# Optimization experiments

Measured on AMD Instinct MI355X. Metric: run time of the kernel, lower is better.

The kernel has to match this reference:

```python
import jax, jax.numpy as jnp
import numpy as np
from jax import lax

B, T, E, H, L, V = 64, 512, 512, 1024, 2, 32000  # batch, seq, d_emb, d_hid, n_layer, n_vocab


def setup_inputs() -> dict:
    key = jax.random.key(0)
    ks = jax.random.split(key, 8)
    s = 0.03  # small init keeps tanh recurrence well-conditioned
    return {
        "src": jax.random.randint(ks[0], (B, T), 0, V),
        "emb_table": jax.random.normal(ks[1], (V, E), jnp.float32) * s,
        "W1": jax.random.normal(ks[2], (H, E), jnp.float32) * s,
        "b1": jnp.zeros((H,), jnp.float32),
        "W2": jax.random.normal(ks[3], (H, H), jnp.float32) * s,
        "b2": jnp.zeros((H,), jnp.float32),
        # layer 0 input dim = H; layers >0 input dim = 2H (bidirectional concat)
        "W_ih0": jax.random.normal(ks[4], (2, H, H), jnp.float32) * s,
        "W_ihL": jax.random.normal(ks[5], (L - 1, 2, H, 2 * H), jnp.float32) * s,
        "W_hh": jax.random.normal(ks[6], (L, 2, H, H), jnp.float32) * s,
        "b_ih": jnp.zeros((L, 2, H), jnp.float32),
        "b_hh": jnp.zeros((L, 2, H), jnp.float32),
    }


def _rnn_dir(x, Wih, Whh, bih, bhh, reverse):
    # x: [B, T, Din]. Precompute input projection as one big GEMM, then scan.
    pre = jnp.einsum('bti,hi->tbh', x, Wih) + bih  # [T, B, H]

    def step(h, p):
        h = jnp.tanh(p + h @ Whh.T + bhh)
        return h, h

    h0 = jnp.zeros((x.shape[0], Whh.shape[0]), x.dtype)
    hT, hs = lax.scan(step, h0, pre, reverse=reverse)
    return hT, jnp.transpose(hs, (1, 0, 2))  # final state [B,H], outputs [B,T,H]


def reference(src, emb_table, W1, b1, W2, b2, W_ih0, W_ihL, W_hh, b_ih, b_hh):
    # Embedding with padding_idx=0 (row zeroed)
    table = emb_table.at[0].set(0.0)
    x = table[src]  # [B, T, E]
    # emb_to_hid MLP (dropout is identity in eval mode)
    x = jax.nn.relu(x @ W1.T + b1)
    x = jax.nn.relu(x @ W2.T + b2)  # [B, T, H]
    finals = []
    inp = x
    for l in range(L):
        Wih = W_ih0 if l == 0 else W_ihL[l - 1]
        hf, of = _rnn_dir(inp, Wih[0], W_hh[l, 0], b_ih[l, 0], b_hh[l, 0], False)
        hb, ob = _rnn_dir(inp, Wih[1], W_hh[l, 1], b_ih[l, 1], b_hh[l, 1], True)
        finals += [hf, hb]
        inp = jnp.concatenate([of, ob], axis=-1)  # [B, T, 2H]
    # torch h_n layout: [n_layer * num_directions, B, H], layer-major, dir-minor
    return jnp.stack(finals, axis=0)
```

## Files before the change

kernel.cpp:

```cpp
#include <hip/hip_runtime.h>


typedef _Float16 f16;
typedef _Float16 f16x8 __attribute__((ext_vector_type(8)));
typedef _Float16 f16x4 __attribute__((ext_vector_type(4)));
typedef float f32x4 __attribute__((ext_vector_type(4)));

static const size_t MB_ = 1024ull * 1024ull;
static const size_t OFF_X0    = 0;
static const size_t OFF_X1    = 64 * MB_;
static const size_t OFF_EMB   = OFF_X1;
static const size_t OFF_MLP1  = 96 * MB_;
static const size_t OFF_H     = 192 * MB_;
static const size_t OFF_FLAGS = 192 * MB_ + 512 * 1024;
static const size_t OFF_BIAS  = 192 * MB_ + 576 * 1024;
static const size_t OFF_W1C   = 193 * MB_;
static const size_t OFF_W2C   = 194 * MB_;
static const size_t WS_NEED   = 196 * MB_;
static const size_t Q_X0     = 0;
static const size_t Q_EMB    = 64 * MB_;
static const size_t Q_MLP1   = 96 * MB_;
static const size_t Q_W1C    = 160 * MB_;
static const size_t Q_W2C    = 161 * MB_;
static const size_t Q_PRE0D0 = 64 * MB_;
static const size_t Q_PRE0D1 = 128 * MB_;
static const size_t Q_HB0    = 192 * MB_;
static const size_t Q_FL0    = 192 * MB_ + 512 * 1024;
static const size_t Q_BIAS0  = 192 * MB_ + 544 * 1024;
static const size_t Q_PRE1D0 = 0;
static const size_t Q_PRE1D1 = 192 * MB_;
static const size_t Q_HB1    = 64 * MB_;
static const size_t Q_FL1    = 64 * MB_ + 512 * 1024;
static const size_t Q_BIAS1  = 64 * MB_ + 544 * 1024;
static const size_t WS_NEED2 = 256 * MB_;

__device__ __forceinline__ void gld16(const void* g, void* l) {
#if __has_builtin(__builtin_amdgcn_global_load_lds)
  __builtin_amdgcn_global_load_lds((const __attribute__((address_space(1))) void*)g,
                                   (__attribute__((address_space(3))) void*)l, 16, 0, 0);
#else
  *(f16x8*)l = *(const f16x8*)g;
#endif
}

__device__ __forceinline__ float tanh_fast(float x) {
  float ax = __builtin_fabsf(x);
  float e = __builtin_amdgcn_exp2f(ax * 2.8853900817779268f);
  float r = 1.0f - 2.0f * __builtin_amdgcn_rcpf(e + 1.0f);
  return __builtin_copysignf(r, x);
}


__global__ void zero_k(unsigned int* __restrict__ p, int n) {
  int i = blockIdx.x * blockDim.x + threadIdx.x;
  if (i < n) p[i] = 0u;
}

__global__ void cvt_k(const float* __restrict__ in, f16* __restrict__ out, int n4) {
  int i = blockIdx.x * blockDim.x + threadIdx.x;
  int stride = gridDim.x * blockDim.x;
  for (; i < n4; i += stride) {
    float4 v = ((const float4*)in)[i];
    f16x4 o = {(f16)v.x, (f16)v.y, (f16)v.z, (f16)v.w};
    ((f16x4*)out)[i] = o;
  }
}

__global__ void bias_k(const float* __restrict__ a, const float* __restrict__ b, float* __restrict__ o) {
  int i = blockIdx.x * blockDim.x + threadIdx.x;
  if (i < 4096) o[i] = a[i] + b[i];
}

__global__ void embed_k(const int* __restrict__ src, const float* __restrict__ tab, f16* __restrict__ out) {
  int m = blockIdx.x;
  int tid = threadIdx.x;
  int tok = src[m];
  f16x4 o = {(f16)0.f, (f16)0.f, (f16)0.f, (f16)0.f};
  if (tok != 0) {
    float4 v = *(const float4*)(tab + (size_t)tok * 512 + tid * 4);
    o[0] = (f16)v.x; o[1] = (f16)v.y; o[2] = (f16)v.z; o[3] = (f16)v.w;
  }
  *(f16x4*)(out + (size_t)m * 512 + tid * 4) = o;
}

template <int EPI>
__global__ __launch_bounds__(256) void gemm_f16(
    const f16* __restrict__ A, int lda, const f16* __restrict__ Bw,
    f16* __restrict__ out, const float* __restrict__ bias, int M, int N, int K) {
  __shared__ alignas(16) f16 As[4096];
  __shared__ alignas(16) f16 Bs[4096];
  const int nt = N >> 7;
  const int bx = blockIdx.x;
  const int tm = bx / nt, tn = bx - tm * nt;
  const int tid = threadIdx.x;
  const int l = tid & 63, w = tid >> 6;
  const int wr = w >> 1, wc = w & 1;
  const int srow = (w << 4) + (l >> 2);
  const int scol = (l & 3) << 3;
  const f16* Ab = A + (size_t)(tm * 128 + srow) * lda + scol;
  const f16* Bb = Bw + (size_t)(tn * 128 + srow) * K + scol;
  f32x4 acc[4][4];
#pragma unroll
  for (int i = 0; i < 4; i++)
#pragma unroll
    for (int j = 0; j < 4; j++) acc[i][j] = (f32x4){0.f, 0.f, 0.f, 0.f};
  const int ar = l & 15, ak = (l >> 4) << 3;
  for (int k0 = 0; k0 < K; k0 += 32) {
    gld16(Ab + k0, &As[tid * 8]);
    gld16(Ab + (size_t)64 * lda + k0, &As[tid * 8 + 2048]);
    gld16(Bb + k0, &Bs[tid * 8]);
    gld16(Bb + (size_t)64 * K + k0, &Bs[tid * 8 + 2048]);
    __syncthreads();
    f16x8 av[4], bv[4];
#pragma unroll
    for (int i = 0; i < 4; i++) av[i] = *(const f16x8*)&As[(wr * 64 + i * 16 + ar) * 32 + ak];
#pragma unroll
    for (int j = 0; j < 4; j++) bv[j] = *(const f16x8*)&Bs[(wc * 64 + j * 16 + ar) * 32 + ak];
#pragma unroll
    for (int i = 0; i < 4; i++)
#pragma unroll
      for (int j = 0; j < 4; j++)
        acc[i][j] = __builtin_amdgcn_mfma_f32_16x16x32_f16(av[i], bv[j], acc[i][j], 0, 0, 0);
    __syncthreads();
  }
  const int r0 = (l >> 4) << 2, c0 = l & 15;
#pragma unroll
  for (int i = 0; i < 4; i++) {
#pragma unroll
    for (int j = 0; j < 4; j++) {
      const int col = tn * 128 + wc * 64 + j * 16 + c0;
      const float bc = (EPI & 1) ? bias[col] : 0.f;
#pragma unroll
      for (int r = 0; r < 4; r++) {
        const int row = tm * 128 + wr * 64 + i * 16 + r0 + r;
        float v = acc[i][j][r];
        if (EPI & 1) { v += bc; v = v > 0.f ? v : 0.f; }
        if (EPI & 2) {
          const int b_ = row >> 9, t = row & 511;
          out[((size_t)(t * 64 + b_) << 10) + col] = (f16)v;
        } else {
          out[(size_t)row * N + col] = (f16)v;
        }
      }
    }
  }
}

__global__ __launch_bounds__(256) void gemm_b32(
    const f16* __restrict__ A, int lda, const float* __restrict__ Bw,
    f16* __restrict__ out, int M, int N, int K) {
  __shared__ alignas(16) f16 As[4096];
  __shared__ alignas(16) f16 Bs[4096];
  const int nt = N >> 7;
  const int bx = blockIdx.x;
  const int tm = bx / nt, tn = bx - tm * nt;
  const int tid = threadIdx.x;
  const int l = tid & 63, w = tid >> 6;
  const int wr = w >> 1, wc = w & 1;
  const int srow = (w << 4) + (l >> 2);
  const int scol = (l & 3) << 3;
  const f16* Ab = A + (size_t)(tm * 128 + srow) * lda + scol;
  const int brow = tid >> 1, bcol = (tid & 1) << 4;
  const float* Bb = Bw + (size_t)(tn * 128 + brow) * K + bcol;
  f32x4 acc[4][4];
#pragma unroll
  for (int i = 0; i < 4; i++)
#pragma unroll
    for (int j = 0; j < 4; j++) acc[i][j] = (f32x4){0.f, 0.f, 0.f, 0.f};
  const int ar = l & 15, ak = (l >> 4) << 3;
  for (int k0 = 0; k0 < K; k0 += 32) {
    gld16(Ab + k0, &As[tid * 8]);
    gld16(Ab + (size_t)64 * lda + k0, &As[tid * 8 + 2048]);
    {
      const float* bp = Bb + k0;
      float4 u0 = *(const float4*)(bp + 0), u1 = *(const float4*)(bp + 4);
      float4 u2 = *(const float4*)(bp + 8), u3 = *(const float4*)(bp + 12);
      f16x8 h0 = {(f16)u0.x, (f16)u0.y, (f16)u0.z, (f16)u0.w,
                  (f16)u1.x, (f16)u1.y, (f16)u1.z, (f16)u1.w};
      f16x8 h1 = {(f16)u2.x, (f16)u2.y, (f16)u2.z, (f16)u2.w,
                  (f16)u3.x, (f16)u3.y, (f16)u3.z, (f16)u3.w};
      *(f16x8*)&Bs[brow * 32 + bcol] = h0;
      *(f16x8*)&Bs[brow * 32 + bcol + 8] = h1;
    }
    __syncthreads();
    f16x8 av[4], bv[4];
#pragma unroll
    for (int i = 0; i < 4; i++) av[i] = *(const f16x8*)&As[(wr * 64 + i * 16 + ar) * 32 + ak];
#pragma unroll
    for (int j = 0; j < 4; j++) bv[j] = *(const f16x8*)&Bs[(wc * 64 + j * 16 + ar) * 32 + ak];
#pragma unroll
    for (int i = 0; i < 4; i++)
#pragma unroll
      for (int j = 0; j < 4; j++)
        acc[i][j] = __builtin_amdgcn_mfma_f32_16x16x32_f16(av[i], bv[j], acc[i][j], 0, 0, 0);
    __syncthreads();
  }
  const int r0 = (l >> 4) << 2, c0 = l & 15;
#pragma unroll
  for (int i = 0; i < 4; i++) {
#pragma unroll
    for (int j = 0; j < 4; j++) {
      const int col = tn * 128 + wc * 64 + j * 16 + c0;
#pragma unroll
      for (int r = 0; r < 4; r++) {
        const int row = tm * 128 + wr * 64 + i * 16 + r0 + r;
        out[(size_t)row * N + col] = (f16)acc[i][j][r];
      }
    }
  }
}

__global__ __launch_bounds__(256) void gemm_b32c(
    const f16* __restrict__ A0, const f16* __restrict__ A1, const float* __restrict__ Bw,
    f16* __restrict__ out, int M, int N) {
  constexpr int K = 2048;
  __shared__ alignas(16) f16 As[4096];
  __shared__ alignas(16) f16 Bs[4096];
  const int nt = N >> 7;
  const int bx = blockIdx.x;
  const int tm = bx / nt, tn = bx - tm * nt;
  const int tid = threadIdx.x;
  const int l = tid & 63, w = tid >> 6;
  const int wr = w >> 1, wc = w & 1;
  const int srow = (w << 4) + (l >> 2);
  const int scol = (l & 3) << 3;
  const int brow = tid >> 1, bcol = (tid & 1) << 4;
  const float* Bb = Bw + (size_t)(tn * 128 + brow) * K + bcol;
  f32x4 acc[4][4];
#pragma unroll
  for (int i = 0; i < 4; i++)
#pragma unroll
    for (int j = 0; j < 4; j++) acc[i][j] = (f32x4){0.f, 0.f, 0.f, 0.f};
  const int ar = l & 15, ak = (l >> 4) << 3;
  for (int k0 = 0; k0 < K; k0 += 32) {
    const f16* base = (k0 < 1024) ? A0 : A1;
    const int ko = k0 & 1023;
    const f16* Ab = base + (size_t)(tm * 128 + srow) * 1024 + ko + scol;
    gld16(Ab, &As[tid * 8]);
    gld16(Ab + (size_t)64 * 1024, &As[tid * 8 + 2048]);
    {
      const float* bp = Bb + k0;
      float4 u0 = *(const float4*)(bp + 0), u1 = *(const float4*)(bp + 4);
      float4 u2 = *(const float4*)(bp + 8), u3 = *(const float4*)(bp + 12);
      f16x8 h0 = {(f16)u0.x, (f16)u0.y, (f16)u0.z, (f16)u0.w,
                  (f16)u1.x, (f16)u1.y, (f16)u1.z, (f16)u1.w};
      f16x8 h1 = {(f16)u2.x, (f16)u2.y, (f16)u2.z, (f16)u2.w,
                  (f16)u3.x, (f16)u3.y, (f16)u3.z, (f16)u3.w};
      *(f16x8*)&Bs[brow * 32 + bcol] = h0;
      *(f16x8*)&Bs[brow * 32 + bcol + 8] = h1;
    }
    __syncthreads();
    f16x8 av[4], bv[4];
#pragma unroll
    for (int i = 0; i < 4; i++) av[i] = *(const f16x8*)&As[(wr * 64 + i * 16 + ar) * 32 + ak];
#pragma unroll
    for (int j = 0; j < 4; j++) bv[j] = *(const f16x8*)&Bs[(wc * 64 + j * 16 + ar) * 32 + ak];
#pragma unroll
    for (int i = 0; i < 4; i++)
#pragma unroll
      for (int j = 0; j < 4; j++)
        acc[i][j] = __builtin_amdgcn_mfma_f32_16x16x32_f16(av[i], bv[j], acc[i][j], 0, 0, 0);
    __syncthreads();
  }
  const int r0 = (l >> 4) << 2, c0 = l & 15;
#pragma unroll
  for (int i = 0; i < 4; i++) {
#pragma unroll
    for (int j = 0; j < 4; j++) {
      const int col = tn * 128 + wc * 64 + j * 16 + c0;
#pragma unroll
      for (int r = 0; r < 4; r++) {
        const int row = tm * 128 + wr * 64 + i * 16 + r0 + r;
        out[(size_t)row * N + col] = (f16)acc[i][j][r];
      }
    }
  }
}

template <int LAYER>
__global__ __launch_bounds__(512, 1) void rnn_scan(
    const f16* __restrict__ X, const float* __restrict__ Wih, const float* __restrict__ Whh,
    const float* __restrict__ bsum, f16* __restrict__ hbuf, unsigned int* __restrict__ flags,
    f16* __restrict__ seqout, float* __restrict__ dout) {
  constexpr int KX = LAYER ? 2048 : 1024;
  constexpr int XSH = LAYER ? 11 : 10;
  constexpr int NKX = KX / 128;
  constexpr int NKH = 8;
  const int bid = blockIdx.x;
  const int g_ = (bid & 7) >> 1;
  const int dir = g_ >> 1, bg = g_ & 1;
  const int cg = ((bid & 1) << 5) | (bid >> 3);
  const int tid = threadIdx.x, l = tid & 63, w = tid >> 6;
  const int mi = w & 1, kq = w >> 1;
  __shared__ alignas(16) f16 Wl[16 * 1024];
  __shared__ alignas(16) f16 Wi[16 * KX];
  __shared__ f32x4 part[2][4][64];
  __shared__ alignas(16) f16 p2[32][16];
  __shared__ unsigned int cnt;
  const int ld = LAYER * 2 + dir;
  if (tid == 0) cnt = 0u;
  for (int ch = tid; ch < 2048; ch += 512) {
    const int n = ch >> 7, k0 = (ch & 127) << 3;
    const float* wp = Whh + (((size_t)(ld * 1024 + cg * 16 + n)) << 10) + k0;
    float4 v0 = *(const float4*)wp, v1 = *(const float4*)(wp + 4);
    f16x8 hv = {(f16)v0.x, (f16)v0.y, (f16)v0.z, (f16)v0.w,
                (f16)v1.x, (f16)v1.y, (f16)v1.z, (f16)v1.w};
    *(f16x8*)&Wl[(n << 10) + (k0 ^ ((n & 7) << 3))] = hv;
  }
  for (int ch = tid; ch < (16 * KX / 8); ch += 512) {
    const int n = ch >> (XSH - 3), k0 = (ch & (KX / 8 - 1)) << 3;
    const float* wp = Wih + ((size_t)(dir * 1024 + cg * 16 + n)) * KX + k0;
    float4 v0 = *(const float4*)wp, v1 = *(const float4*)(wp + 4);
    f16x8 hv = {(f16)v0.x, (f16)v0.y, (f16)v0.z, (f16)v0.w,
                (f16)v1.x, (f16)v1.y, (f16)v1.z, (f16)v1.w};
    *(f16x8*)&Wi[(n << XSH) + (k0 ^ ((n & 7) << 3))] = hv;
  }
  const float bn = bsum[(ld << 10) + cg * 16 + (l & 15)];
  f16* hD = hbuf + ((size_t)dir << 17);
  unsigned int* fl = flags + ((dir * 2 + bg) << 10);
  const int arow = bg * 32 + mi * 16 + (l & 15);
  const int akh = (kq << 8) + ((l >> 4) << 3);
  const int akx = kq * (KX / 4) + ((l >> 4) << 3);
  const int wn = l & 15;
  const int wsw = (wn & 7) << 3;

  f16x8 xv[NKX];
  {
    const int t0 = dir ? 511 : 0;
    const f16* xr = X + (((size_t)(t0 * 64 + arow)) << XSH) + akx;
#pragma unroll
    for (int i = 0; i < NKX; i++)
      asm volatile("global_load_dwordx4 %0, %1, off offset:%2"
                   : "=&v"(xv[i]) : "v"(xr), "i"(64 * i));
  }
  __syncthreads();

  for (int s = 0; s < 512; ++s) {
    const int t = dir ? (511 - s) : s;
    f32x4 acc = {0.f, 0.f, 0.f, 0.f};
    if (s > 0) {
      if (w == 7) {
        const unsigned int tgt = (unsigned int)(LAYER * 512 + s);
        unsigned int* fp = fl + l * 16;
        for (;;) {
          unsigned int f = __hip_atomic_load(fp, __ATOMIC_RELAXED, __HIP_MEMORY_SCOPE_AGENT);
          if (__all((int)(f >= tgt))) break;
        }
      }
      __syncthreads();
      const f16* hrow = hD + (((size_t)(s & 1)) << 16) + (((size_t)arow) << 10) + akh;
      f16x8 hv[NKH];
#pragma unroll
      for (int i = 0; i < NKH; i++)
        asm volatile("global_load_dwordx4 %0, %1, off offset:%2 sc0 sc1"
                     : "=&v"(hv[i]) : "v"(hrow), "i"(64 * i));
      asm volatile("s_waitcnt vmcnt(%0)" :: "i"(NKH) : "memory");
      __builtin_amdgcn_sched_barrier(0);
#pragma unroll
      for (int it = 0; it < NKX; ++it) {
        const int ko = akx + it * 32;
        f16x8 bv = *(const f16x8*)&Wi[(wn << XSH) + (ko ^ wsw)];
        acc = __builtin_amdgcn_mfma_f32_16x16x32_f16(xv[it], bv, acc, 0, 0, 0);
      }
      asm volatile("s_waitcnt vmcnt(0)" ::: "memory");
      __builtin_amdgcn_sched_barrier(0);
#pragma unroll
      for (int it = 0; it < NKH; ++it) {
        const int ko = akh + it * 32;
        f16x8 bv = *(const f16x8*)&Wl[(wn << 10) + (ko ^ wsw)];
        acc = __builtin_amdgcn_mfma_f32_16x16x32_f16(hv[it], bv, acc, 0, 0, 0);
      }
    } else {
      asm volatile("s_waitcnt vmcnt(0)" ::: "memory");
      __builtin_amdgcn_sched_barrier(0);
#pragma unroll
      for (int it = 0; it < NKX; ++it) {
        const int ko = akx + it * 32;
        f16x8 bv = *(const f16x8*)&Wi[(wn << XSH) + (ko ^ wsw)];
        acc = __builtin_amdgcn_mfma_f32_16x16x32_f16(xv[it], bv, acc, 0, 0, 0);
      }
    }
    part[mi][kq][l] = acc;
    __syncthreads();
    if (w < 2) {
      f32x4 sum = part[w][0][l];
      sum += part[w][1][l];
      sum += part[w][2][l];
      sum += part[w][3][l];
#pragma unroll
      for (int r = 0; r < 4; ++r) {
        const int row = ((l >> 4) << 2) + r;
        float v = tanh_fast(sum[r] + bn);
        p2[(w << 4) + row][l & 15] = (f16)v;
        if (s == 511) {
          const int b_ = bg * 32 + (w << 4) + row;
          dout[(((size_t)(ld * 64 + b_)) << 10) + cg * 16 + (l & 15)] = v;
        }
      }
      asm volatile("s_waitcnt lgkmcnt(0)" ::: "memory");
      __builtin_amdgcn_sched_barrier(0);
      if (l < 32) {
        const int rr = (w << 4) + (l >> 1), hf = l & 1;
        f16x8 pv = *(const f16x8*)&p2[rr][hf * 8];
        const int b_ = bg * 32 + rr;
        f16* hp = hD + (((size_t)((s + 1) & 1)) << 16) + (((size_t)b_) << 10) + cg * 16 + hf * 8;
        asm volatile("global_store_dwordx4 %0, %1, off sc0 sc1" :: "v"(hp), "v"(pv) : "memory");
        if (LAYER == 0) {
          f16* sp = seqout + (((size_t)(t * 64 + b_)) << 11) + (dir << 10) + cg * 16 + hf * 8;
          asm volatile("global_store_dwordx4 %0, %1, off" :: "v"(sp), "v"(pv) : "memory");
        }
      }
      asm volatile("s_waitcnt vmcnt(0)" ::: "memory");
      __builtin_amdgcn_sched_barrier(0);
      if (l == 0) {
        unsigned int old = __hip_atomic_fetch_add(&cnt, 1u, __ATOMIC_RELAXED,
                                                  __HIP_MEMORY_SCOPE_WORKGROUP);
        if (old == (unsigned int)(2 * s + 1))
          __hip_atomic_store(&fl[cg * 16], (unsigned int)(LAYER * 512 + s + 1),
                             __ATOMIC_RELAXED, __HIP_MEMORY_SCOPE_AGENT);
      }
    }
    if (s + 1 < 512) {
      const int tn_ = dir ? (511 - (s + 1)) : (s + 1);
      const f16* xr = X + (((size_t)(tn_ * 64 + arow)) << XSH) + akx;
#pragma unroll
      for (int i = 0; i < NKX; i++)
        asm volatile("global_load_dwordx4 %0, %1, off offset:%2"
                     : "=&v"(xv[i]) : "v"(xr), "i"(64 * i));
    }
  }
}

template <int LAYER>
__global__ __launch_bounds__(512, 1) void rnn_scan_pre(
    f16* __restrict__ PRE0, f16* __restrict__ PRE1,
    const float* __restrict__ Whh, const float* __restrict__ bsum,
    f16* __restrict__ hbuf, unsigned int* __restrict__ flags,
    float* __restrict__ dout) {
  constexpr int NKH = 8;
  const int bid = blockIdx.x;
  const int g_ = (bid & 7) >> 1;
  const int dir = g_ >> 1, bg = g_ & 1;
  const int cg = ((bid & 1) << 5) | (bid >> 3);
  const int tid = threadIdx.x, l = tid & 63, w = tid >> 6;
  const int mi = w & 1, kq = w >> 1;
  __shared__ alignas(16) f16 Wl[16 * 1024];
  __shared__ f32x4 part[2][4][64];
  __shared__ alignas(16) f16 p2[32][16];
  __shared__ unsigned int cnt;
  const int ld = LAYER * 2 + dir;
  if (tid == 0) cnt = 0u;
  for (int ch = tid; ch < 2048; ch += 512) {
    const int n = ch >> 7, k0 = (ch & 127) << 3;
    const float* wp = Whh + (((size_t)(ld * 1024 + cg * 16 + n)) << 10) + k0;
    float4 v0 = *(const float4*)wp, v1 = *(const float4*)(wp + 4);
    f16x8 hv = {(f16)v0.x, (f16)v0.y, (f16)v0.z, (f16)v0.w,
                (f16)v1.x, (f16)v1.y, (f16)v1.z, (f16)v1.w};
    *(f16x8*)&Wl[(n << 10) + (k0 ^ ((n & 7) << 3))] = hv;
  }
  const int pcol = cg * 16 + (l & 15);
  const float bn = bsum[(ld << 10) + pcol];
  f16* preD = dir ? PRE1 : PRE0;
  f16* hD = hbuf + ((size_t)dir << 17);
  unsigned int* fl = flags + ((dir * 2 + bg) << 10);
  const int arow = bg * 32 + mi * 16 + (l & 15);
  const int akh = (kq << 8) + ((l >> 4) << 3);
  const int wn = l & 15;
  const int wsw = (wn & 7) << 3;
  const int prow = bg * 32 + (w << 4) + ((l >> 4) << 2);

  unsigned int pu0 = 0, pu1 = 0, pu2 = 0, pu3 = 0;
  if (w < 2) {
    const int t0 = dir ? 511 : 0;
    const f16* ppA = preD + (((size_t)(t0 * 64 + prow)) << 10) + pcol;
    const f16* ppB = ppA + 2048;
    asm volatile("global_load_ushort %0, %1, off" : "=&v"(pu0) : "v"(ppA));
    asm volatile("global_load_ushort %0, %1, off offset:2048" : "=&v"(pu1) : "v"(ppA));
    asm volatile("global_load_ushort %0, %1, off" : "=&v"(pu2) : "v"(ppB));
    asm volatile("global_load_ushort %0, %1, off offset:2048" : "=&v"(pu3) : "v"(ppB));
  }
  __syncthreads();

  for (int s = 0; s < 512; ++s) {
    const int t = dir ? (511 - s) : s;
    f32x4 acc = {0.f, 0.f, 0.f, 0.f};
    if (s > 0) {
      if (w == 7) {
        const unsigned int tgt = (unsigned int)s;
        unsigned int* fp = fl + l * 16;
        for (;;) {
          unsigned int f = __hip_atomic_load(fp, __ATOMIC_RELAXED, __HIP_MEMORY_SCOPE_AGENT);
          if (__all((int)(f >= tgt))) break;
        }
      }
      __syncthreads();
      const f16* hrow = hD + (((size_t)(s & 1)) << 16) + (((size_t)arow) << 10) + akh;
      f16x8 hv[NKH];
#pragma unroll
      for (int i = 0; i < NKH; i++)
        asm volatile("global_load_dwordx4 %0, %1, off offset:%2 sc0 sc1"
                     : "=&v"(hv[i]) : "v"(hrow), "i"(64 * i));
      asm volatile("s_waitcnt vmcnt(0)" ::: "memory");
      __builtin_amdgcn_sched_barrier(0);
#pragma unroll
      for (int it = 0; it < NKH; ++it) {
        const int ko = akh + it * 32;
        f16x8 bv = *(const f16x8*)&Wl[(wn << 10) + (ko ^ wsw)];
        acc = __builtin_amdgcn_mfma_f32_16x16x32_f16(hv[it], bv, acc, 0, 0, 0);
      }
    }
    part[mi][kq][l] = acc;
    __syncthreads();
    if (w < 2) {
      asm volatile("s_waitcnt vmcnt(0)" ::: "memory");
      __builtin_amdgcn_sched_barrier(0);
      float pva[4];
      pva[0] = (float)__builtin_bit_cast(f16, (unsigned short)pu0);
      pva[1] = (float)__builtin_bit_cast(f16, (unsigned short)pu1);
      pva[2] = (float)__builtin_bit_cast(f16, (unsigned short)pu2);
      pva[3] = (float)__builtin_bit_cast(f16, (unsigned short)pu3);
      f32x4 sum = part[w][0][l];
      sum += part[w][1][l];
      sum += part[w][2][l];
      sum += part[w][3][l];
#pragma unroll
      for (int r = 0; r < 4; ++r) {
        const int row = ((l >> 4) << 2) + r;
        float v = tanh_fast(sum[r] + pva[r] + bn);
        p2[(w << 4) + row][l & 15] = (f16)v;
        if (s == 511) {
          const int b_ = bg * 32 + (w << 4) + row;
          dout[(((size_t)(ld * 64 + b_)) << 10) + pcol] = v;
        }
      }
      asm volatile("s_waitcnt lgkmcnt(0)" ::: "memory");
      __builtin_amdgcn_sched_barrier(0);
      if (l < 32) {
        const int rr = (w << 4) + (l >> 1), hf = l & 1;
        f16x8 pv = *(const f16x8*)&p2[rr][hf * 8];
        const int b_ = bg * 32 + rr;
        f16* hp = hD + (((size_t)((s + 1) & 1)) << 16) + (((size_t)b_) << 10) + cg * 16 + hf * 8;
        asm volatile("global_store_dwordx4 %0, %1, off sc0 sc1" :: "v"(hp), "v"(pv) : "memory");
        if (LAYER == 0) {
          f16* xp = preD + (((size_t)(t * 64 + b_)) << 10) + cg * 16 + hf * 8;
          asm volatile("global_store_dwordx4 %0, %1, off" :: "v"(xp), "v"(pv) : "memory");
        }
      }
      asm volatile("s_waitcnt vmcnt(0)" ::: "memory");
      __builtin_amdgcn_sched_barrier(0);
      if (l == 0) {
        unsigned int old = __hip_atomic_fetch_add(&cnt, 1u, __ATOMIC_RELAXED,
                                                  __HIP_MEMORY_SCOPE_WORKGROUP);
        if (old == (unsigned int)(2 * s + 1))
          __hip_atomic_store(&fl[cg * 16], (unsigned int)(s + 1),
                             __ATOMIC_RELAXED, __HIP_MEMORY_SCOPE_AGENT);
      }
      if (s + 1 < 512) {
        const int tn_ = dir ? (511 - (s + 1)) : (s + 1);
        const f16* ppA = preD + (((size_t)(tn_ * 64 + prow)) << 10) + pcol;
        const f16* ppB = ppA + 2048;
        asm volatile("global_load_ushort %0, %1, off" : "=&v"(pu0) : "v"(ppA));
        asm volatile("global_load_ushort %0, %1, off offset:2048" : "=&v"(pu1) : "v"(ppA));
        asm volatile("global_load_ushort %0, %1, off" : "=&v"(pu2) : "v"(ppB));
        asm volatile("global_load_ushort %0, %1, off offset:2048" : "=&v"(pu3) : "v"(ppB));
      }
    }
  }
}


extern "C" void kernel_launch(void* const* d_in, const int* in_sizes, int n_in,
                              void* d_out, int out_size, void* d_ws, size_t ws_size,
                              hipStream_t stream) {
  const int* src    = (const int*)d_in[0];
  const float* emb  = (const float*)d_in[1];
  const float* W1   = (const float*)d_in[2];
  const float* b1   = (const float*)d_in[3];
  const float* W2   = (const float*)d_in[4];
  const float* b2   = (const float*)d_in[5];
  const float* Wih0 = (const float*)d_in[6];
  const float* WihL = (const float*)d_in[7];
  const float* Whh  = (const float*)d_in[8];
  const float* bih  = (const float*)d_in[9];
  const float* bhh  = (const float*)d_in[10];
  float* out = (float*)d_out;
  char* ws = (char*)d_ws;

  if (ws_size < WS_NEED) {
    zero_k<<<(out_size + 255) / 256, 256, 0, stream>>>((unsigned int*)d_out, out_size);
    return;
  }

  if (ws_size >= WS_NEED2) {
    f16* X0    = (f16*)(ws + Q_X0);
    f16* EMB   = (f16*)(ws + Q_EMB);
    f16* MLP1  = (f16*)(ws + Q_MLP1);
    f16* W1C   = (f16*)(ws + Q_W1C);
    f16* W2C   = (f16*)(ws + Q_W2C);
    f16* PRE0D0 = (f16*)(ws + Q_PRE0D0);
    f16* PRE0D1 = (f16*)(ws + Q_PRE0D1);
    f16* HB0   = (f16*)(ws + Q_HB0);
    unsigned int* FL0 = (unsigned int*)(ws + Q_FL0);
    float* BIAS0 = (float*)(ws + Q_BIAS0);
    f16* PRE1D0 = (f16*)(ws + Q_PRE1D0);
    f16* PRE1D1 = (f16*)(ws + Q_PRE1D1);
    f16* HB1   = (f16*)(ws + Q_HB1);
    unsigned int* FL1 = (unsigned int*)(ws + Q_FL1);
    float* BIAS1 = (float*)(ws + Q_BIAS1);

    cvt_k<<<256, 256, 0, stream>>>(W1, W1C, 131072);
    cvt_k<<<256, 256, 0, stream>>>(W2, W2C, 262144);

    embed_k<<<32768, 128, 0, stream>>>(src, emb, EMB);
    gemm_f16<1><<<2048, 256, 0, stream>>>(EMB, 512, W1C, MLP1, b1, 32768, 1024, 512);
    gemm_f16<3><<<2048, 256, 0, stream>>>(MLP1, 1024, W2C, X0, b2, 32768, 1024, 1024);

    gemm_b32<<<2048, 256, 0, stream>>>(X0, 1024, Wih0, PRE0D0, 32768, 1024, 1024);
    gemm_b32<<<2048, 256, 0, stream>>>(X0, 1024, Wih0 + (1u << 20), PRE0D1, 32768, 1024, 1024);
    zero_k<<<16, 256, 0, stream>>>(FL0, 4096);
    bias_k<<<16, 256, 0, stream>>>(bih, bhh, BIAS0);
    rnn_scan_pre<0><<<256, 512, 0, stream>>>(PRE0D0, PRE0D1, Whh, BIAS0, HB0, FL0, out);

    gemm_b32c<<<2048, 256, 0, stream>>>(PRE0D0, PRE0D1, WihL, PRE1D0, 32768, 1024);
    gemm_b32c<<<2048, 256, 0, stream>>>(PRE0D0, PRE0D1, WihL + (1u << 21), PRE1D1, 32768, 1024);
    zero_k<<<16, 256, 0, stream>>>(FL1, 4096);
    bias_k<<<16, 256, 0, stream>>>(bih, bhh, BIAS1);
    rnn_scan_pre<1><<<256, 512, 0, stream>>>(PRE1D0, PRE1D1, Whh, BIAS1, HB1, FL1, out);
    return;
  }

  f16* X0   = (f16*)(ws + OFF_X0);
  f16* X1   = (f16*)(ws + OFF_X1);
  f16* EMB  = (f16*)(ws + OFF_EMB);
  f16* MLP1 = (f16*)(ws + OFF_MLP1);
  f16* HB   = (f16*)(ws + OFF_H);
  unsigned int* FLAGS = (unsigned int*)(ws + OFF_FLAGS);
  float* BIAS = (float*)(ws + OFF_BIAS);
  f16* W1C  = (f16*)(ws + OFF_W1C);
  f16* W2C  = (f16*)(ws + OFF_W2C);

  cvt_k<<<256, 256, 0, stream>>>(W1, W1C, 131072);
  cvt_k<<<256, 256, 0, stream>>>(W2, W2C, 262144);
  bias_k<<<16, 256, 0, stream>>>(bih, bhh, BIAS);
  zero_k<<<16, 256, 0, stream>>>(FLAGS, 4096);

  embed_k<<<32768, 128, 0, stream>>>(src, emb, EMB);
  gemm_f16<1><<<2048, 256, 0, stream>>>(EMB, 512, W1C, MLP1, b1, 32768, 1024, 512);
  gemm_f16<3><<<2048, 256, 0, stream>>>(MLP1, 1024, W2C, X0, b2, 32768, 1024, 1024);

  rnn_scan<0><<<256, 512, 0, stream>>>(X0, Wih0, Whh, BIAS, HB, FLAGS, X1, out);
  rnn_scan<1><<<256, 512, 0, stream>>>(X1, WihL, Whh, BIAS, HB, FLAGS, nullptr, out);
}
```

Measured before the change: 4.999 ms.

## Drop K-split in recurrent scan: two waves compute full K, no LDS reduction

The recurrent scan kernel moves from 8 waves that split the K dimension four ways, with a shared-memory partial-sum reduction, to 4 waves where only two compute the full 1024-wide dot product. Each of those two waves issues all 32 hidden-state loads up front and consumes them in staged waits. This removes the LDS partial write, one block barrier and the reduction from each serial step. In exchange, the per-step MFMA chain per wave is four times longer and register pressure rises from holding 32 f16x8 vectors.

```diff
diff --git a/kernel.cpp b/kernel.cpp
--- a/kernel.cpp
+++ b/kernel.cpp
@@ -432,25 +432,22 @@
 }
 
 template <int LAYER>
-__global__ __launch_bounds__(512, 1) void rnn_scan_pre(
+__global__ __launch_bounds__(256, 1) void rnn_scan_pre(
     f16* __restrict__ PRE0, f16* __restrict__ PRE1,
     const float* __restrict__ Whh, const float* __restrict__ bsum,
     f16* __restrict__ hbuf, unsigned int* __restrict__ flags,
     float* __restrict__ dout) {
-  constexpr int NKH = 8;
   const int bid = blockIdx.x;
   const int g_ = (bid & 7) >> 1;
   const int dir = g_ >> 1, bg = g_ & 1;
   const int cg = ((bid & 1) << 5) | (bid >> 3);
   const int tid = threadIdx.x, l = tid & 63, w = tid >> 6;
-  const int mi = w & 1, kq = w >> 1;
   __shared__ alignas(16) f16 Wl[16 * 1024];
-  __shared__ f32x4 part[2][4][64];
   __shared__ alignas(16) f16 p2[32][16];
   __shared__ unsigned int cnt;
   const int ld = LAYER * 2 + dir;
   if (tid == 0) cnt = 0u;
-  for (int ch = tid; ch < 2048; ch += 512) {
+  for (int ch = tid; ch < 2048; ch += 256) {
     const int n = ch >> 7, k0 = (ch & 127) << 3;
     const float* wp = Whh + (((size_t)(ld * 1024 + cg * 16 + n)) << 10) + k0;
     float4 v0 = *(const float4*)wp, v1 = *(const float4*)(wp + 4);
@@ -463,8 +460,8 @@
   f16* preD = dir ? PRE1 : PRE0;
   f16* hD = hbuf + ((size_t)dir << 17);
   unsigned int* fl = flags + ((dir * 2 + bg) << 10);
-  const int arow = bg * 32 + mi * 16 + (l & 15);
-  const int akh = (kq << 8) + ((l >> 4) << 3);
+  const int arow = bg * 32 + (w << 4) + (l & 15);
+  const int kb = (l >> 4) << 3;
   const int wn = l & 15;
   const int wsw = (wn & 7) << 3;
   const int prow = bg * 32 + (w << 4) + ((l >> 4) << 2);
@@ -485,7 +482,7 @@
     const int t = dir ? (511 - s) : s;
     f32x4 acc = {0.f, 0.f, 0.f, 0.f};
     if (s > 0) {
-      if (w == 7) {
+      if (w == 3) {
         const unsigned int tgt = (unsigned int)s;
         unsigned int* fp = fl + l * 16;
         for (;;) {
@@ -494,23 +491,47 @@
         }
       }
       __syncthreads();
-      const f16* hrow = hD + (((size_t)(s & 1)) << 16) + (((size_t)arow) << 10) + akh;
-      f16x8 hv[NKH];
-#pragma unroll
-      for (int i = 0; i < NKH; i++)
-        asm volatile("global_load_dwordx4 %0, %1, off offset:%2 sc0 sc1"
-                     : "=&v"(hv[i]) : "v"(hrow), "i"(64 * i));
-      asm volatile("s_waitcnt vmcnt(0)" ::: "memory");
-      __builtin_amdgcn_sched_barrier(0);
-#pragma unroll
-      for (int it = 0; it < NKH; ++it) {
-        const int ko = akh + it * 32;
-        f16x8 bv = *(const f16x8*)&Wl[(wn << 10) + (ko ^ wsw)];
-        acc = __builtin_amdgcn_mfma_f32_16x16x32_f16(hv[it], bv, acc, 0, 0, 0);
-      }
-    }
-    part[mi][kq][l] = acc;
-    __syncthreads();
+      if (w < 2) {
+        const f16* hrow = hD + (((size_t)(s & 1)) << 16) + (((size_t)arow) << 10) + kb;
+        f16x8 hv[32];
+#pragma unroll
+        for (int i = 0; i < 32; i++)
+          asm volatile("global_load_dwordx4 %0, %1, off offset:%2 sc0 sc1"
+                       : "=&v"(hv[i]) : "v"(hrow), "i"(64 * i));
+        asm volatile("s_waitcnt vmcnt(24)" ::: "memory");
+        __builtin_amdgcn_sched_barrier(0);
+#pragma unroll
+        for (int it = 0; it < 8; ++it) {
+          const int ko = kb + it * 32;
+          f16x8 bv = *(const f16x8*)&Wl[(wn << 10) + (ko ^ wsw)];
+          acc = __builtin_amdgcn_mfma_f32_16x16x32_f16(hv[it], bv, acc, 0, 0, 0);
+        }
+        asm volatile("s_waitcnt vmcnt(16)" ::: "memory");
+        __builtin_amdgcn_sched_barrier(0);
+#pragma unroll
+        for (int it = 8; it < 16; ++it) {
+          const int ko = kb + it * 32;
+          f16x8 bv = *(const f16x8*)&Wl[(wn << 10) + (ko ^ wsw)];
+          acc = __builtin_amdgcn_mfma_f32_16x16x32_f16(hv[it], bv, acc, 0, 0, 0);
+        }
+        asm volatile("s_waitcnt vmcnt(8)" ::: "memory");
+        __builtin_amdgcn_sched_barrier(0);
+#pragma unroll
+        for (int it = 16; it < 24; ++it) {
+          const int ko = kb + it * 32;
+          f16x8 bv = *(const f16x8*)&Wl[(wn << 10) + (ko ^ wsw)];
+          acc = __builtin_amdgcn_mfma_f32_16x16x32_f16(hv[it], bv, acc, 0, 0, 0);
+        }
+        asm volatile("s_waitcnt vmcnt(0)" ::: "memory");
+        __builtin_amdgcn_sched_barrier(0);
+#pragma unroll
+        for (int it = 24; it < 32; ++it) {
+          const int ko = kb + it * 32;
+          f16x8 bv = *(const f16x8*)&Wl[(wn << 10) + (ko ^ wsw)];
+          acc = __builtin_amdgcn_mfma_f32_16x16x32_f16(hv[it], bv, acc, 0, 0, 0);
+        }
+      }
+    }
     if (w < 2) {
       asm volatile("s_waitcnt vmcnt(0)" ::: "memory");
       __builtin_amdgcn_sched_barrier(0);
@@ -519,14 +540,10 @@
       pva[1] = (float)__builtin_bit_cast(f16, (unsigned short)pu1);
       pva[2] = (float)__builtin_bit_cast(f16, (unsigned short)pu2);
       pva[3] = (float)__builtin_bit_cast(f16, (unsigned short)pu3);
-      f32x4 sum = part[w][0][l];
-      sum += part[w][1][l];
-      sum += part[w][2][l];
-      sum += part[w][3][l];
 #pragma unroll
       for (int r = 0; r < 4; ++r) {
         const int row = ((l >> 4) << 2) + r;
-        float v = tanh_fast(sum[r] + pva[r] + bn);
+        float v = tanh_fast(acc[r] + pva[r] + bn);
         p2[(w << 4) + row][l & 15] = (f16)v;
         if (s == 511) {
           const int b_ = bg * 32 + (w << 4) + row;
@@ -619,13 +636,13 @@
     gemm_b32<<<2048, 256, 0, stream>>>(X0, 1024, Wih0 + (1u << 20), PRE0D1, 32768, 1024, 1024);
     zero_k<<<16, 256, 0, stream>>>(FL0, 4096);
     bias_k<<<16, 256, 0, stream>>>(bih, bhh, BIAS0);
-    rnn_scan_pre<0><<<256, 512, 0, stream>>>(PRE0D0, PRE0D1, Whh, BIAS0, HB0, FL0, out);
+    rnn_scan_pre<0><<<256, 256, 0, stream>>>(PRE0D0, PRE0D1, Whh, BIAS0, HB0, FL0, out);
 
     gemm_b32c<<<2048, 256, 0, stream>>>(PRE0D0, PRE0D1, WihL, PRE1D0, 32768, 1024);
     gemm_b32c<<<2048, 256, 0, stream>>>(PRE0D0, PRE0D1, WihL + (1u << 21), PRE1D1, 32768, 1024);
     zero_k<<<16, 256, 0, stream>>>(FL1, 4096);
     bias_k<<<16, 256, 0, stream>>>(bih, bhh, BIAS1);
-    rnn_scan_pre<1><<<256, 512, 0, stream>>>(PRE1D0, PRE1D1, Whh, BIAS1, HB1, FL1, out);
+    rnn_scan_pre<1><<<256, 256, 0, stream>>>(PRE1D0, PRE1D1, Whh, BIAS1, HB1, FL1, out);
     return;
   }
 
```

New measurement: 4.771 ms, median of 2. 1.05x faster.
